# Kernel tuning notes

Hardware: AMD Instinct MI355X
Metric: run time of the kernel (lower is better)

## Reference

```python
import jax, jax.numpy as jnp
import numpy as np

B, S, E, H, Dh = 2, 2048, 1024, 16, 64


def setup_inputs() -> dict:
    key = jax.random.key(0)
    ks = jax.random.split(key, 8)
    w = 0.02
    return {
        "x": jax.random.normal(ks[0], (B, S, E), jnp.float32),
        # torch Linear convention: weight (out, in) = (Dh, E), stacked over heads
        "Wq": jax.random.normal(ks[1], (H, Dh, E), jnp.float32) * w,
        "bq": jax.random.normal(ks[2], (H, Dh), jnp.float32) * w,
        "Wk": jax.random.normal(ks[3], (H, Dh, E), jnp.float32) * w,
        "bk": jax.random.normal(ks[4], (H, Dh), jnp.float32) * w,
        "Wv": jax.random.normal(ks[5], (H, Dh, E), jnp.float32) * w,
        "bv": jax.random.normal(ks[6], (H, Dh), jnp.float32) * w,
        "proj": jax.random.normal(ks[7], (H * Dh, E), jnp.float32) * w,
    }


def reference(x, Wq, bq, Wk, bk, Wv, bv, proj):
    b, s, e = x.shape
    h, dh, _ = Wq.shape
    scale = jnp.sqrt(jnp.asarray(dh, x.dtype))
    # per-head linear projections: y = x @ W.T + b  -> (b, h, s, dh)
    q = jnp.einsum('bse,hde->bhsd', x, Wq) + bq[None, :, None, :]
    k = jnp.einsum('bse,hde->bhsd', x, Wk) + bk[None, :, None, :]
    v = jnp.einsum('bse,hde->bhsd', x, Wv) + bv[None, :, None, :]
    causal = jnp.triu(jnp.ones((s, s), bool), 1)
    scores = jnp.einsum('bhsd,bhtd->bhst', q, k) / scale
    scores = jnp.where(causal[None, None], -jnp.inf, scores)
    # quirk: softmax output divided by sqrt(head_size) a second time
    att = jax.nn.softmax(scores, axis=-1) / scale
    z = jnp.einsum('bhst,bhtd->bhsd', att, v)
    # quirk: torch reshapes (B,H,S,Dh) row-major into (B,S,H*Dh) WITHOUT transpose
    z = z.reshape(b, s, h * dh)
    return z @ proj
```

## Files before the change

kernel.cpp:

```cpp
#include <hip/hip_runtime.h>
#include <hip/hip_bf16.h>

typedef unsigned short u16;
typedef unsigned int u32;
typedef __bf16 bf16x8 __attribute__((ext_vector_type(8)));
typedef float f32x4 __attribute__((ext_vector_type(4)));
typedef u16 u16x8 __attribute__((ext_vector_type(8)));
typedef u16 u16x4 __attribute__((ext_vector_type(4)));
typedef u32 u32x4 __attribute__((ext_vector_type(4)));

#define B_ 2
#define S_ 2048
#define E_ 1024
#define H_ 16
#define Dh_ 64

static __device__ __forceinline__ u16 f2bf(float f) {
  unsigned u = __builtin_bit_cast(unsigned, f);
  u += 0x7fff + ((u >> 16) & 1);
  return (u16)(u >> 16);
}

static __device__ __forceinline__ void gload16(const u16* g, u16* l) {
  __builtin_amdgcn_global_load_lds((const __attribute__((address_space(1))) unsigned int*)g,
                                   (__attribute__((address_space(3))) unsigned int*)l,
                                   16, 0, 0);
}

__global__ void cvt_all(const float* __restrict__ x, const float* __restrict__ wq,
                        const float* __restrict__ wk, const float* __restrict__ wv,
                        u16* __restrict__ xb, u16* __restrict__ wcat) {
  const int i = blockIdx.x * 256 + threadIdx.x;
  const float* src; u16x8* dst;
  if (i < 524288) {
    src = x + (size_t)i * 8;            dst = (u16x8*)xb + i;
  } else {
    const int j = i - 524288;
    dst = (u16x8*)wcat + j;
    if (j < 131072)      src = wq + (size_t)j * 8;
    else if (j < 262144) src = wk + (size_t)(j - 131072) * 8;
    else                 src = wv + (size_t)(j - 262144) * 8;
  }
  float4 a = ((const float4*)src)[0], b = ((const float4*)src)[1];
  u16x8 o;
  o[0] = f2bf(a.x); o[1] = f2bf(a.y); o[2] = f2bf(a.z); o[3] = f2bf(a.w);
  o[4] = f2bf(b.x); o[5] = f2bf(b.y); o[6] = f2bf(b.z); o[7] = f2bf(b.w);
  *dst = o;
}

__global__ void transpose_cvt(const float* __restrict__ in, u16* __restrict__ outT) {
  __shared__ float t[32][33];
  const int e = blockIdx.x * 32 + threadIdx.x;
  const int f = blockIdx.y * 32 + threadIdx.y;
  t[threadIdx.y][threadIdx.x] = in[f * 1024 + e];
  __syncthreads();
  const int eo = blockIdx.x * 32 + threadIdx.y;
  const int fo = blockIdx.y * 32 + threadIdx.x;
  outT[eo * 1024 + fo] = f2bf(t[threadIdx.x][threadIdx.y]);
}

__global__ __launch_bounds__(512, 2) void qkv_gemm(const u16* __restrict__ Wcat,
                                                   const u16* __restrict__ Xm,
                                                   const float* __restrict__ bq,
                                                   const float* __restrict__ bk,
                                                   const float* __restrict__ bv,
                                                   u16* __restrict__ Qb, u16* __restrict__ Kb,
                                                   u16* __restrict__ Vtb, float qs) {
  __shared__ __align__(16) u16 Alds[2][16384];
  __shared__ __align__(16) u16 Blds[2][16384];
  const int tid = threadIdx.x;
  const int wv = tid >> 6, ln = tid & 63;
  const int lq = ln & 15, lg = ln >> 4;
  const int wm = wv >> 2, wn = wv & 3;
  const int bid = blockIdx.x;
  const int xcd = bid & 7, w = bid >> 3;
  const int bx = w % 12;
  const int by = xcd * 2 + w / 12;
  const int ra0 = bx * 256, rb0 = by * 256;

  const int r_t = tid >> 3, c_t = tid & 7;
  const int gcol = (c_t ^ (r_t & 7)) * 8;
  const u16* Asrc = Wcat + (ra0 + r_t) * 1024 + gcol;
  const u16* Bsrc = Xm   + (rb0 + r_t) * 1024 + gcol;

  const int sc0 = (lg ^ (lq & 7)) * 8;
  const int sc1 = ((4 + lg) ^ (lq & 7)) * 8;
  const int baseA = (wm * 128 + lq) * 64;
  const int baseB = (wn * 64 + lq) * 64;

  f32x4 acc[8][4];
  const f32x4 z4 = {0.f, 0.f, 0.f, 0.f};
#pragma unroll
  for (int i = 0; i < 8; ++i)
#pragma unroll
    for (int j = 0; j < 4; ++j) acc[i][j] = z4;

#define SA(Q, KT, BUF) gload16(Asrc + (Q) * 65536 + (KT) * 64, &Alds[BUF][((Q) * 512 + tid) * 8])
#define SB(Q, KT, BUF) gload16(Bsrc + (Q) * 65536 + (KT) * 64, &Blds[BUF][((Q) * 512 + tid) * 8])
#define LOADA(MH, SC) do {                                                         \
    _Pragma("unroll") for (int ii = 0; ii < 4; ++ii)                               \
      af[ii] = *(const bf16x8*)&Alds[cb][baseA + (MH) * 4096 + ii * 1024 + (SC)];  \
  } while (0)
#define LOADB(DST, SC) do {                                                        \
    _Pragma("unroll") for (int j = 0; j < 4; ++j)                                  \
      DST[j] = *(const bf16x8*)&Blds[cb][baseB + j * 1024 + (SC)];                 \
  } while (0)
#define MF(MH, BQ) do {                                                            \
    _Pragma("unroll") for (int ii = 0; ii < 4; ++ii)                               \
      _Pragma("unroll") for (int j = 0; j < 4; ++j)                                \
        acc[(MH) * 4 + ii][j] =                                                    \
            __builtin_amdgcn_mfma_f32_16x16x32_bf16(af[ii], BQ[j],                 \
                                                    acc[(MH) * 4 + ii][j], 0, 0, 0); \
  } while (0)

  SB(0, 0, 0); SB(1, 0, 0); SB(2, 0, 0); SB(3, 0, 0);
  SA(0, 0, 0); SA(2, 0, 0); SA(1, 0, 0); SA(3, 0, 0);

  for (int kt = 0; kt < 16; ++kt) {
    const int cb = kt & 1, nb = cb ^ 1;
    const bool st = (kt < 15);
    asm volatile("s_waitcnt vmcnt(2)" ::: "memory");
    __builtin_amdgcn_s_barrier();
    __builtin_amdgcn_sched_barrier(0);
    bf16x8 af[4], bq0[4], bq1[4];
    LOADA(0, sc0);
    LOADB(bq0, sc0);
    if (st) { SB(0, kt + 1, nb); SB(1, kt + 1, nb); }
    __builtin_amdgcn_s_barrier();
    asm volatile("s_waitcnt lgkmcnt(0)" ::: "memory");
    __builtin_amdgcn_sched_barrier(0);
    __builtin_amdgcn_s_setprio(1);
    MF(0, bq0);
    __builtin_amdgcn_s_setprio(0);
    __builtin_amdgcn_s_barrier();
    LOADA(0, sc1);
    LOADB(bq1, sc1);
    if (st) { SB(2, kt + 1, nb); SB(3, kt + 1, nb); }
    __builtin_amdgcn_s_barrier();
    asm volatile("s_waitcnt lgkmcnt(0)" ::: "memory");
    __builtin_amdgcn_sched_barrier(0);
    __builtin_amdgcn_s_setprio(1);
    MF(0, bq1);
    __builtin_amdgcn_s_setprio(0);
    __builtin_amdgcn_s_barrier();
    if (st) { asm volatile("s_waitcnt vmcnt(4)" ::: "memory"); }
    else    { asm volatile("s_waitcnt vmcnt(0)" ::: "memory"); }
    __builtin_amdgcn_s_barrier();
    __builtin_amdgcn_sched_barrier(0);
    LOADA(1, sc0);
    if (st) { SA(0, kt + 1, nb); SA(2, kt + 1, nb); }
    __builtin_amdgcn_s_barrier();
    asm volatile("s_waitcnt lgkmcnt(0)" ::: "memory");
    __builtin_amdgcn_sched_barrier(0);
    __builtin_amdgcn_s_setprio(1);
    MF(1, bq0);
    __builtin_amdgcn_s_setprio(0);
    __builtin_amdgcn_s_barrier();
    LOADA(1, sc1);
    if (st) { SA(1, kt + 1, nb); SA(3, kt + 1, nb); }
    __builtin_amdgcn_s_barrier();
    asm volatile("s_waitcnt lgkmcnt(0)" ::: "memory");
    __builtin_amdgcn_sched_barrier(0);
    __builtin_amdgcn_s_setprio(1);
    MF(1, bq1);
    __builtin_amdgcn_s_setprio(0);
    __builtin_amdgcn_s_barrier();
  }
#undef SA
#undef SB
#undef LOADA
#undef LOADB
#undef MF

  const int region = bx >> 2;
  const float* bias = (region == 0) ? bq : (region == 1) ? bk : bv;
  const float osc = (region == 0) ? qs : 1.0f;
#pragma unroll
  for (int i = 0; i < 8; ++i) {
#pragma unroll
    for (int j = 0; j < 4; ++j) {
      const int n0 = ra0 + wm * 128 + (i >> 2) * 64 + (i & 3) * 16 + lg * 4;
      const int nl = n0 & 1023;
      const int h = nl >> 6, d = nl & 63;
      const int m = rb0 + wn * 64 + j * 16 + lq;
      const int bb = m >> 11, s = m & 2047;
      const float4 b4 = *(const float4*)&bias[nl];
      if (region < 2) {
        u16* out = (region == 0) ? Qb : Kb;
        u16x4 pk;
        pk[0] = f2bf((acc[i][j][0] + b4.x) * osc);
        pk[1] = f2bf((acc[i][j][1] + b4.y) * osc);
        pk[2] = f2bf((acc[i][j][2] + b4.z) * osc);
        pk[3] = f2bf((acc[i][j][3] + b4.w) * osc);
        *(u16x4*)&out[((bb * H_ + h) * S_ + s) * Dh_ + d] = pk;
      } else {
        const float bvv[4] = {b4.x, b4.y, b4.z, b4.w};
#pragma unroll
        for (int r = 0; r < 4; ++r)
          Vtb[((bb * H_ + h) * Dh_ + d + r) * S_ + s] = f2bf(acc[i][j][r] + bvv[r]);
      }
    }
  }
}

__global__ __launch_bounds__(256) void proj_gemm(const u16* __restrict__ Am,
                                                 const u16* __restrict__ Bm,
                                                 float* __restrict__ out) {
  __shared__ __align__(16) u16 As[2][4096];
  __shared__ __align__(16) u16 Bs[2][2048];
  const int tid = threadIdx.x;
  const int wv = tid >> 6, ln = tid & 63;
  const int lq = ln & 15, lg = ln >> 4;
  const int bid = blockIdx.x;
  const int xcd = bid & 7, within = bid >> 3;
  const int bx = within & 7;
  const int by = xcd * 8 + (within >> 3);
  const int ra0 = bx * 128, rb0 = by * 64;
  const int wra = wv >> 1, wrb = wv & 1;

  f32x4 acc[4][2];
  const f32x4 z4 = {0.f, 0.f, 0.f, 0.f};
#pragma unroll
  for (int i = 0; i < 4; ++i)
#pragma unroll
    for (int j = 0; j < 2; ++j) acc[i][j] = z4;

  const int arow = tid >> 2;
  const int acol = (tid & 3) * 8;
  const int brow = wv * 16 + (ln >> 2);
  const int bcol = (ln & 3) * 8;
  const u16* Ags = Am + (ra0 + arow) * 1024 + acol;
  const u16* Bgs = Bm + (rb0 + brow) * 1024 + bcol;

#define PSTAGE(KT, BUF) do { const int k0_ = (KT) * 32;              \
    gload16(Ags + k0_,         &As[BUF][wv * 512]);                  \
    gload16(Ags + 65536 + k0_, &As[BUF][wv * 512 + 2048]);           \
    gload16(Bgs + k0_,         &Bs[BUF][wv * 512]); } while (0)

  PSTAGE(0, 0);
  for (int kt = 0; kt < 32; ++kt) {
    const int cb = kt & 1;
    if (kt < 31) {
      PSTAGE(kt + 1, cb ^ 1);
      asm volatile("s_waitcnt vmcnt(3)" ::: "memory");
    } else {
      asm volatile("s_waitcnt vmcnt(0)" ::: "memory");
    }
    __builtin_amdgcn_s_barrier();
    __builtin_amdgcn_sched_barrier(0);
    bf16x8 af[4], bfr[2];
#pragma unroll
    for (int i = 0; i < 4; ++i)
      af[i] = *(const bf16x8*)&As[cb][(wra * 64 + i * 16 + lq) * 32 + lg * 8];
#pragma unroll
    for (int j = 0; j < 2; ++j)
      bfr[j] = *(const bf16x8*)&Bs[cb][(wrb * 32 + j * 16 + lq) * 32 + lg * 8];
#pragma unroll
    for (int i = 0; i < 4; ++i)
#pragma unroll
      for (int j = 0; j < 2; ++j)
        acc[i][j] = __builtin_amdgcn_mfma_f32_16x16x32_bf16(af[i], bfr[j], acc[i][j], 0, 0, 0);
    __builtin_amdgcn_sched_barrier(0);
    __builtin_amdgcn_s_barrier();
  }
#undef PSTAGE

  const int Ar = ra0 + wra * 64, Br = rb0 + wrb * 32;
#pragma unroll
  for (int i = 0; i < 4; ++i)
#pragma unroll
    for (int j = 0; j < 2; ++j) {
      const int e0 = Ar + i * 16 + lg * 4;
      const int m = Br + j * 16 + lq;
      *(f32x4*)&out[m * 1024 + e0] = acc[i][j];
    }
}

__global__ __launch_bounds__(512, 4) void attn_kernel(const u16* __restrict__ Q,
                                                      const u16* __restrict__ K,
                                                      const u16* __restrict__ Vt,
                                                      u16* __restrict__ Z) {
  __shared__ __align__(16) u16 Ktile[2][8192];
  __shared__ __align__(16) u16 Vtile[2][8192];
  const int tid = threadIdx.x;
  const int wv = tid >> 6, ln = tid & 63;
  const int lq = ln & 15, lg = ln >> 4;
  const bool lgodd = (lg & 1) != 0;
  const int id = blockIdx.x;
  const int within = id >> 3;
  const int xg = id & 7;
  int bh, qt;
  if (within < 32) { bh = xg * 4 + (within >> 4);     qt = 15 - (within & 15); }
  else { const int w = within - 32; bh = xg * 4 + 2 + (w >> 4); qt = w & 15; }
  const int qrow = (qt << 7) + wv * 16 + lq;
  const u16* Qp = Q + (size_t)bh * S_ * Dh_;
  const u16* Kp = K + (size_t)bh * S_ * Dh_;
  const u16* Vp = Vt + (size_t)bh * Dh_ * S_;

  int kgofs[2], vgrow[2], vgcol[2];
#pragma unroll
  for (int j = 0; j < 2; ++j) {
    const int p = j * 512 + tid;
    const int gk = p ^ ((p >> 3) & 7);
    kgofs[j] = (gk >> 3) * 64 + (gk & 7) * 8;
    vgrow[j] = p >> 4;
    vgcol[j] = ((p & 15) ^ ((p >> 4) & 15)) * 8;
  }
  const int sc0 = (lg ^ (lq & 7)) * 8;
  const int sc1 = ((4 + lg) ^ (lq & 7)) * 8;

  bf16x8 qf0 = *(const bf16x8*)&Qp[qrow * Dh_ + lg * 8];
  bf16x8 qf1 = *(const bf16x8*)&Qp[qrow * Dh_ + 32 + lg * 8];

  f32x4 o[4];
  const f32x4 z4 = {0.f, 0.f, 0.f, 0.f};
#pragma unroll
  for (int dt = 0; dt < 4; ++dt) o[dt] = z4;
  float l_lane = 0.f;

#define STAGE(KT, BUF) do { const int kb_ = (KT) * 128;                              \
    gload16(Kp + (size_t)kb_ * 64 + kgofs[0], &Ktile[BUF][wv * 512]);                \
    gload16(Kp + (size_t)kb_ * 64 + kgofs[1], &Ktile[BUF][4096 + wv * 512]);         \
    gload16(Vp + (size_t)vgrow[0] * 2048 + kb_ + vgcol[0], &Vtile[BUF][wv * 512]);   \
    gload16(Vp + (size_t)vgrow[1] * 2048 + kb_ + vgcol[1], &Vtile[BUF][4096 + wv * 512]); \
  } while (0)

  STAGE(0, 0);

  int cur = 0;
  for (int kt = 0; kt <= qt; ++kt) {
    if (kt < qt) {
      STAGE(kt + 1, cur ^ 1);
      asm volatile("s_waitcnt vmcnt(4)" ::: "memory");
    } else {
      asm volatile("s_waitcnt vmcnt(0)" ::: "memory");
    }
    __builtin_amdgcn_s_barrier();
    __builtin_amdgcn_sched_barrier(0);
    const int k0 = kt * 128;
    const bool diag = (kt == qt);
    const int nkk = diag ? ((wv >> 1) + 1) : 4;
#pragma unroll
    for (int kk = 0; kk < 4; ++kk) {
      if (kk < nkk) {
        const int rA = (kk * 32 + lq) * 64;
        const int rB = rA + 1024;
        bf16x8 kA0 = *(const bf16x8*)&Ktile[cur][rA + sc0];
        bf16x8 kA1 = *(const bf16x8*)&Ktile[cur][rA + sc1];
        bf16x8 kB0 = *(const bf16x8*)&Ktile[cur][rB + sc0];
        bf16x8 kB1 = *(const bf16x8*)&Ktile[cur][rB + sc1];
        f32x4 sa = z4, sb = z4;
        __builtin_amdgcn_s_setprio(1);
        sa = __builtin_amdgcn_mfma_f32_16x16x32_bf16(kA0, qf0, sa, 0, 0, 0);
        sa = __builtin_amdgcn_mfma_f32_16x16x32_bf16(kA1, qf1, sa, 0, 0, 0);
        sb = __builtin_amdgcn_mfma_f32_16x16x32_bf16(kB0, qf0, sb, 0, 0, 0);
        sb = __builtin_amdgcn_mfma_f32_16x16x32_bf16(kB1, qf1, sb, 0, 0, 0);
        __builtin_amdgcn_s_setprio(0);
        if (diag) {
          const int keyA = k0 + kk * 32 + lg * 4;
          const int keyB = keyA + 16;
#pragma unroll
          for (int r = 0; r < 4; ++r) {
            if (keyA + r > qrow) sa[r] = -3.0e38f;
            if (keyB + r > qrow) sb[r] = -3.0e38f;
          }
        }
        float e0 = __builtin_amdgcn_exp2f(sa[0]);
        float e1 = __builtin_amdgcn_exp2f(sa[1]);
        float e2 = __builtin_amdgcn_exp2f(sa[2]);
        float e3 = __builtin_amdgcn_exp2f(sa[3]);
        float f0 = __builtin_amdgcn_exp2f(sb[0]);
        float f1 = __builtin_amdgcn_exp2f(sb[1]);
        float f2 = __builtin_amdgcn_exp2f(sb[2]);
        float f3 = __builtin_amdgcn_exp2f(sb[3]);
        l_lane += ((e0 + e1) + (e2 + e3)) + ((f0 + f1) + (f2 + f3));
        u32 A0, A1, B0, B1;
        asm("v_cvt_pk_bf16_f32 %0, %1, %2" : "=v"(A0) : "v"(e0), "v"(e1));
        asm("v_cvt_pk_bf16_f32 %0, %1, %2" : "=v"(A1) : "v"(e2), "v"(e3));
        asm("v_cvt_pk_bf16_f32 %0, %1, %2" : "=v"(B0) : "v"(f0), "v"(f1));
        asm("v_cvt_pk_bf16_f32 %0, %1, %2" : "=v"(B1) : "v"(f2), "v"(f3));
        asm("v_permlane32_swap_b32 %0, %1" : "+v"(A0), "+v"(B0));
        asm("v_permlane32_swap_b32 %0, %1" : "+v"(A1), "+v"(B1));
        const u32 A0x = __shfl_xor((int)A0, 16), B0x = __shfl_xor((int)B0, 16);
        const u32 A1x = __shfl_xor((int)A1, 16), B1x = __shfl_xor((int)B1, 16);
        u32x4 w;
        w[0] = lgodd ? B0x : A0;
        w[1] = lgodd ? B1x : A1;
        w[2] = lgodd ? B0 : A0x;
        w[3] = lgodd ? B1 : A1x;
        const bf16x8 pf = __builtin_bit_cast(bf16x8, w);
        const int scvk = ((kk * 4 + lg) ^ lq) * 8;
        __builtin_amdgcn_s_setprio(1);
#pragma unroll
        for (int dt = 0; dt < 4; ++dt) {
          bf16x8 vf = *(const bf16x8*)&Vtile[cur][(dt * 16 + lq) * 128 + scvk];
          o[dt] = __builtin_amdgcn_mfma_f32_16x16x32_bf16(vf, pf, o[dt], 0, 0, 0);
        }
        __builtin_amdgcn_s_setprio(0);
      }
    }
    __builtin_amdgcn_sched_barrier(0);
    __builtin_amdgcn_s_barrier();
    cur ^= 1;
  }
#undef STAGE

  float l = l_lane;
  l += __shfl_xor(l, 16);
  l += __shfl_xor(l, 32);
  const float inv = 0.125f / l;
#pragma unroll
  for (int dt = 0; dt < 4; ++dt) {
    u16x4 pko;
#pragma unroll
    for (int r = 0; r < 4; ++r) pko[r] = f2bf(o[dt][r] * inv);
    *(u16x4*)&Z[((size_t)bh * S_ + qrow) * Dh_ + dt * 16 + lg * 4] = pko;
  }
}

extern "C" void kernel_launch(void* const* d_in, const int* in_sizes, int n_in,
                              void* d_out, int out_size, void* d_ws, size_t ws_size,
                              hipStream_t stream) {
  const float* x    = (const float*)d_in[0];
  const float* Wq   = (const float*)d_in[1];
  const float* bq   = (const float*)d_in[2];
  const float* Wk   = (const float*)d_in[3];
  const float* bk   = (const float*)d_in[4];
  const float* Wv   = (const float*)d_in[5];
  const float* bv   = (const float*)d_in[6];
  const float* proj = (const float*)d_in[7];
  float* out = (float*)d_out;

  char* p = (char*)d_ws;
  u16* xb   = (u16*)p; p += (size_t)4096 * 1024 * 2;
  u16* wcat = (u16*)p; p += (size_t)3072 * 1024 * 2;
  u16* pjt  = (u16*)p; p += (size_t)1024 * 1024 * 2;
  u16* Qb   = (u16*)p; p += (size_t)4096 * 1024 * 2;
  u16* Kb   = (u16*)p; p += (size_t)4096 * 1024 * 2;
  u16* Vtb  = (u16*)p; p += (size_t)4096 * 1024 * 2;
  u16* Zb   = (u16*)p; p += (size_t)4096 * 1024 * 2;

  cvt_all<<<dim3(3584), dim3(256), 0, stream>>>(x, Wq, Wk, Wv, xb, wcat);
  transpose_cvt<<<dim3(32, 32), dim3(32, 32), 0, stream>>>(proj, pjt);

  const float qs = 0.125f * 1.44269504f;
  qkv_gemm<<<dim3(192), dim3(512), 0, stream>>>(wcat, xb, bq, bk, bv, Qb, Kb, Vtb, qs);

  attn_kernel<<<dim3(512), dim3(512), 0, stream>>>(Qb, Kb, Vtb, Zb);

  proj_gemm<<<dim3(512), dim3(256), 0, stream>>>(pjt, Zb, out);
}
```

Before: 104.6 us.

## Restructure double-buffer loops to single barrier per iteration with prefetch after barrier

In all three kernels (QKV GEMM, output projection GEMM, attention), each loop iteration now waits on vmcnt(0), does one barrier, and only then issues the next tile's global-to-LDS prefetch into the other buffer. This replaces the finer interleaved barrier/waitcnt pattern and drops the trailing end-of-iteration barrier. The intent is to remove barrier and synchronisation overhead. The cost is that the prefetch overlaps less with compute, since each iteration waits for all outstanding loads. The projection GEMM also gains setprio around its MFMA block.

```diff
diff --git a/kernel.cpp b/kernel.cpp
--- a/kernel.cpp
+++ b/kernel.cpp
@@ -114,57 +114,36 @@
   } while (0)
 
   SB(0, 0, 0); SB(1, 0, 0); SB(2, 0, 0); SB(3, 0, 0);
-  SA(0, 0, 0); SA(2, 0, 0); SA(1, 0, 0); SA(3, 0, 0);
+  SA(0, 0, 0); SA(1, 0, 0); SA(2, 0, 0); SA(3, 0, 0);
 
   for (int kt = 0; kt < 16; ++kt) {
     const int cb = kt & 1, nb = cb ^ 1;
-    const bool st = (kt < 15);
-    asm volatile("s_waitcnt vmcnt(2)" ::: "memory");
+    asm volatile("s_waitcnt vmcnt(0)" ::: "memory");
     __builtin_amdgcn_s_barrier();
     __builtin_amdgcn_sched_barrier(0);
+    if (kt < 15) {
+      SB(0, kt + 1, nb); SB(1, kt + 1, nb); SB(2, kt + 1, nb); SB(3, kt + 1, nb);
+      SA(0, kt + 1, nb); SA(1, kt + 1, nb); SA(2, kt + 1, nb); SA(3, kt + 1, nb);
+    }
     bf16x8 af[4], bq0[4], bq1[4];
+    LOADB(bq0, sc0);
+    LOADB(bq1, sc1);
     LOADA(0, sc0);
-    LOADB(bq0, sc0);
-    if (st) { SB(0, kt + 1, nb); SB(1, kt + 1, nb); }
-    __builtin_amdgcn_s_barrier();
-    asm volatile("s_waitcnt lgkmcnt(0)" ::: "memory");
-    __builtin_amdgcn_sched_barrier(0);
     __builtin_amdgcn_s_setprio(1);
     MF(0, bq0);
     __builtin_amdgcn_s_setprio(0);
-    __builtin_amdgcn_s_barrier();
     LOADA(0, sc1);
-    LOADB(bq1, sc1);
-    if (st) { SB(2, kt + 1, nb); SB(3, kt + 1, nb); }
-    __builtin_amdgcn_s_barrier();
-    asm volatile("s_waitcnt lgkmcnt(0)" ::: "memory");
-    __builtin_amdgcn_sched_barrier(0);
     __builtin_amdgcn_s_setprio(1);
     MF(0, bq1);
     __builtin_amdgcn_s_setprio(0);
-    __builtin_amdgcn_s_barrier();
-    if (st) { asm volatile("s_waitcnt vmcnt(4)" ::: "memory"); }
-    else    { asm volatile("s_waitcnt vmcnt(0)" ::: "memory"); }
-    __builtin_amdgcn_s_barrier();
-    __builtin_amdgcn_sched_barrier(0);
     LOADA(1, sc0);
-    if (st) { SA(0, kt + 1, nb); SA(2, kt + 1, nb); }
-    __builtin_amdgcn_s_barrier();
-    asm volatile("s_waitcnt lgkmcnt(0)" ::: "memory");
-    __builtin_amdgcn_sched_barrier(0);
     __builtin_amdgcn_s_setprio(1);
     MF(1, bq0);
     __builtin_amdgcn_s_setprio(0);
-    __builtin_amdgcn_s_barrier();
     LOADA(1, sc1);
-    if (st) { SA(1, kt + 1, nb); SA(3, kt + 1, nb); }
-    __builtin_amdgcn_s_barrier();
-    asm volatile("s_waitcnt lgkmcnt(0)" ::: "memory");
-    __builtin_amdgcn_sched_barrier(0);
     __builtin_amdgcn_s_setprio(1);
     MF(1, bq1);
     __builtin_amdgcn_s_setprio(0);
-    __builtin_amdgcn_s_barrier();
   }
 #undef SA
 #undef SB
@@ -240,14 +219,10 @@
   PSTAGE(0, 0);
   for (int kt = 0; kt < 32; ++kt) {
     const int cb = kt & 1;
-    if (kt < 31) {
-      PSTAGE(kt + 1, cb ^ 1);
-      asm volatile("s_waitcnt vmcnt(3)" ::: "memory");
-    } else {
-      asm volatile("s_waitcnt vmcnt(0)" ::: "memory");
-    }
+    asm volatile("s_waitcnt vmcnt(0)" ::: "memory");
     __builtin_amdgcn_s_barrier();
     __builtin_amdgcn_sched_barrier(0);
+    if (kt < 31) PSTAGE(kt + 1, cb ^ 1);
     bf16x8 af[4], bfr[2];
 #pragma unroll
     for (int i = 0; i < 4; ++i)
@@ -255,13 +230,13 @@
 #pragma unroll
     for (int j = 0; j < 2; ++j)
       bfr[j] = *(const bf16x8*)&Bs[cb][(wrb * 32 + j * 16 + lq) * 32 + lg * 8];
+    __builtin_amdgcn_s_setprio(1);
 #pragma unroll
     for (int i = 0; i < 4; ++i)
 #pragma unroll
       for (int j = 0; j < 2; ++j)
         acc[i][j] = __builtin_amdgcn_mfma_f32_16x16x32_bf16(af[i], bfr[j], acc[i][j], 0, 0, 0);
-    __builtin_amdgcn_sched_barrier(0);
-    __builtin_amdgcn_s_barrier();
+    __builtin_amdgcn_s_setprio(0);
   }
 #undef PSTAGE
 
@@ -329,14 +304,10 @@
 
   int cur = 0;
   for (int kt = 0; kt <= qt; ++kt) {
-    if (kt < qt) {
-      STAGE(kt + 1, cur ^ 1);
-      asm volatile("s_waitcnt vmcnt(4)" ::: "memory");
-    } else {
-      asm volatile("s_waitcnt vmcnt(0)" ::: "memory");
-    }
+    asm volatile("s_waitcnt vmcnt(0)" ::: "memory");
     __builtin_amdgcn_s_barrier();
     __builtin_amdgcn_sched_barrier(0);
+    if (kt < qt) STAGE(kt + 1, cur ^ 1);
     const int k0 = kt * 128;
     const bool diag = (kt == qt);
     const int nkk = diag ? ((wv >> 1) + 1) : 4;
@@ -399,8 +370,6 @@
         __builtin_amdgcn_s_setprio(0);
       }
     }
-    __builtin_amdgcn_sched_barrier(0);
-    __builtin_amdgcn_s_barrier();
     cur ^= 1;
   }
 #undef STAGE
```

After: 107.7 us. +3.0%, slower.
